# Kernel optimization log

Hardware: AMD Instinct MI355X
Metric: run time of the kernel (lower is better)

Reference implementation:

```python
import jax, jax.numpy as jnp
import numpy as np

TAU = 0.08


def setup_inputs() -> dict:
    key = jax.random.key(0)
    k1, k2 = jax.random.split(key)
    pos_waves = jax.random.normal(k1, (32, 64, 8192), dtype=jnp.float32)
    neg_waves = jax.random.normal(k2, (32, 64, 8192), dtype=jnp.float32)
    return {"pos_waves": pos_waves, "neg_waves": neg_waves}


def _normalize(w):
    # global min/max over the whole wave tensor (matches torch.min/torch.max on 2D tensor)
    lo = jnp.min(w, axis=(1, 2), keepdims=True)  # [N,1,1]
    hi = jnp.max(w, axis=(1, 2), keepdims=True)
    return (w - lo) / (hi - lo)


def _pairwise_negpearson(X, Y):
    # X: [N,B,T], Y: [M,B,T] -> mean over B of (1 - pearson) for every (n,m) pair
    T = X.shape[-1]
    sx = jnp.sum(X, axis=-1)            # [N,B]
    sy = jnp.sum(Y, axis=-1)            # [M,B]
    sx2 = jnp.sum(X * X, axis=-1)       # [N,B]
    sy2 = jnp.sum(Y * Y, axis=-1)       # [M,B]
    sxy = jnp.einsum('nbt,mbt->nmb', X, Y)  # [N,M,B]
    num = T * sxy - sx[:, None, :] * sy[None, :, :]
    den = jnp.sqrt((T * sx2 - sx * sx)[:, None, :] * (T * sy2 - sy * sy)[None, :, :])
    return jnp.mean(1.0 - num / den, axis=-1)  # [N,M]


def reference(pos_waves, neg_waves):
    P = _normalize(pos_waves)   # [N,B,T]
    Q = _normalize(neg_waves)   # [M,B,T]
    N = P.shape[0]

    d_pp = _pairwise_negpearson(P, P)                    # [N,N]
    upper = jnp.triu(jnp.ones((N, N), dtype=bool), k=1)  # i < j pairs only
    pos_total = jnp.sum(jnp.where(upper, jnp.exp(d_pp / TAU), 0.0))

    d_pn = _pairwise_negpearson(P, Q)                    # [N,M]
    neg_total = jnp.sum(jnp.exp(d_pn / TAU))

    return jnp.log10(pos_total / neg_total + 1.0)
```

## Files before the change

### kernel.cpp

```cpp
#include <hip/hip_runtime.h>
#include <cmath>

#define N_ 32
#define B_ 64
#define T_ 8192
#define CPB 16
#define PSTRIDE 2176
#define PAIRF 260
#define TENSF 4160
#define LDSB  33280

typedef _Float16 half8 __attribute__((ext_vector_type(8)));
typedef float floatx4 __attribute__((ext_vector_type(4)));

__global__ __launch_bounds__(512, 8) void k_stage1(const float* __restrict__ pos,
                                                   const float* __restrict__ neg,
                                                   float* __restrict__ partial) {
    __shared__ __align__(16) float smem[LDSB / 4];

    const int bid = blockIdx.x;
    const int b = bid >> 4, c = bid & 15;
    const int tid = threadIdx.x;
    const int wave = tid >> 6, lane = tid & 63;

    const int tzw = wave >> 2;
    const int quad = wave & 3;
    const float* gsrc = tzw ? neg : pos;
    const float* gptr[4];
    int ldsoff[4];
#pragma unroll
    for (int j = 0; j < 4; ++j) {
        int p = quad * 4 + j;
        int row = 2 * p + (lane >> 5);
        gptr[j] = gsrc + ((long)(row * B_ + b)) * T_ + c * 512 + (lane & 31) * 4;
        ldsoff[j] = tzw * TENSF + p * PAIRF;
    }

    const int mat = wave >> 2, qi = (wave >> 1) & 1, qj = wave & 1;
    const int m16 = lane & 15, h2 = lane >> 4;
    const int arow = qi * 16 + m16, brow = qj * 16 + m16;
    const float* aptr = smem + ((arow >> 1) * PAIRF + (arow & 1) * 128);
    const float* bptr = smem + mat * TENSF + ((brow >> 1) * PAIRF + (brow & 1) * 128);

    const int stream = tid >> 3, sub = tid & 7;
    const int srow = stream & 31, stz = stream >> 5;
    const float* sptr = smem + stz * TENSF + ((srow >> 1) * PAIRF + (srow & 1) * 128) + sub * 16;

    floatx4 acc = {};
    float ssum = 0.f, ssq = 0.f;

    for (int ch = 0; ch < 4; ++ch) {
#pragma unroll
        for (int j = 0; j < 4; ++j) {
            __builtin_amdgcn_global_load_lds(
                (const __attribute__((address_space(1))) void*)(gptr[j] + ch * 128),
                (__attribute__((address_space(3))) void*)(smem + ldsoff[j]), 16, 0, 0);
        }
        asm volatile("s_waitcnt vmcnt(0)" ::: "memory");
        __syncthreads();

#pragma unroll
        for (int kk = 0; kk < 4; ++kk) {
            const int t0 = kk * 32 + h2 * 8;
            float4 a0 = *(const float4*)(aptr + t0);
            float4 a1 = *(const float4*)(aptr + t0 + 4);
            float4 b0 = *(const float4*)(bptr + t0);
            float4 b1 = *(const float4*)(bptr + t0 + 4);
            half8 af = {(_Float16)a0.x, (_Float16)a0.y, (_Float16)a0.z, (_Float16)a0.w,
                        (_Float16)a1.x, (_Float16)a1.y, (_Float16)a1.z, (_Float16)a1.w};
            half8 bf = {(_Float16)b0.x, (_Float16)b0.y, (_Float16)b0.z, (_Float16)b0.w,
                        (_Float16)b1.x, (_Float16)b1.y, (_Float16)b1.z, (_Float16)b1.w};
            acc = __builtin_amdgcn_mfma_f32_16x16x32_f16(af, bf, acc, 0, 0, 0);
        }

#pragma unroll
        for (int f = 0; f < 4; ++f) {
            float4 v = *(const float4*)(sptr + f * 4);
            ssum += v.x + v.y + v.z + v.w;
            ssq = fmaf(v.x, v.x, ssq); ssq = fmaf(v.y, v.y, ssq);
            ssq = fmaf(v.z, v.z, ssq); ssq = fmaf(v.w, v.w, ssq);
        }

        __syncthreads();
    }

    ssum += __shfl_xor(ssum, 1); ssum += __shfl_xor(ssum, 2); ssum += __shfl_xor(ssum, 4);
    ssq += __shfl_xor(ssq, 1); ssq += __shfl_xor(ssq, 2); ssq += __shfl_xor(ssq, 4);

    float* out = partial + (long)bid * PSTRIDE;
    if (sub == 0) out[2048 + (stz * 2 + 0) * 32 + srow] = ssum;
    if (sub == 1) out[2048 + (stz * 2 + 1) * 32 + srow] = ssq;

#pragma unroll
    for (int reg = 0; reg < 4; ++reg) {
        int rr = qi * 16 + h2 * 4 + reg;
        int cc = qj * 16 + m16;
        out[mat * 1024 + rr * 32 + cc] = acc[reg];
    }
}

__global__ void k_reduce(const float* __restrict__ partial, float* __restrict__ red) {
    const int b = blockIdx.y;
    const int o = blockIdx.x * 128 + threadIdx.x;
    const float* in = partial + (long)b * CPB * PSTRIDE;
    float s = 0.f;
#pragma unroll
    for (int c = 0; c < CPB; ++c) s += in[c * PSTRIDE + o];
    red[(long)b * PSTRIDE + o] = s;
}

__global__ void k_entries(const float* __restrict__ red, double* __restrict__ blocksums) {
    const int tid = threadIdx.x;
    const int w = tid >> 6, lane = tid & 63;
    const int entry = blockIdx.x * 4 + w;
    const int mat = entry >> 10;
    const int idx = entry & 1023;
    const int n = idx >> 5, m = idx & 31;

    const float* rb = red + (long)lane * PSTRIDE;
    float g = rb[mat * 1024 + idx];
    float sxn = rb[2048 + n];
    float sx2n = rb[2080 + n];
    float sym, sy2m;
    if (mat == 0) {
        sym = rb[2048 + m];
        sy2m = rb[2080 + m];
    } else {
        sym = rb[2112 + m];
        sy2m = rb[2144 + m];
    }

    double num = (double)T_ * (double)g - (double)sxn * (double)sym;
    double vx = (double)T_ * (double)sx2n - (double)sxn * (double)sxn;
    double vy = (double)T_ * (double)sy2m - (double)sym * (double)sym;
    double contrib = 1.0 - num / sqrt(vx * vy);

#pragma unroll
    for (int off = 32; off; off >>= 1) contrib += __shfl_down(contrib, off);

    __shared__ double s_pos[4], s_neg[4];
    if (lane == 0) {
        double d = contrib * (1.0 / B_);
        double term = exp(d / 0.08);
        double p = 0.0, q = 0.0;
        if (mat == 0) {
            if (n < m) p = term;
        } else {
            q = term;
        }
        s_pos[w] = p;
        s_neg[w] = q;
    }
    __syncthreads();
    if (tid == 0) {
        blocksums[blockIdx.x * 2 + 0] = s_pos[0] + s_pos[1] + s_pos[2] + s_pos[3];
        blocksums[blockIdx.x * 2 + 1] = s_neg[0] + s_neg[1] + s_neg[2] + s_neg[3];
    }
}

__global__ void k_final(const double* __restrict__ blocksums, float* __restrict__ out) {
    __shared__ double sp[256], sn[256];
    const int tid = threadIdx.x;
    double p = 0.0, q = 0.0;
    for (int i = tid; i < 512; i += 256) {
        p += blocksums[2 * i + 0];
        q += blocksums[2 * i + 1];
    }
    sp[tid] = p;
    sn[tid] = q;
    __syncthreads();
    for (int s = 128; s; s >>= 1) {
        if (tid < s) {
            sp[tid] += sp[tid + s];
            sn[tid] += sn[tid + s];
        }
        __syncthreads();
    }
    if (tid == 0) out[0] = (float)log10(sp[0] / sn[0] + 1.0);
}

extern "C" void kernel_launch(void* const* d_in, const int* in_sizes, int n_in,
                              void* d_out, int out_size, void* d_ws, size_t ws_size,
                              hipStream_t stream) {
    const float* pos = (const float*)d_in[0];
    const float* neg = (const float*)d_in[1];
    float* out = (float*)d_out;

    char* ws = (char*)d_ws;
    float* partial = (float*)ws;
    float* red = (float*)(ws + (size_t)1024 * PSTRIDE * 4);
    double* blocksums = (double*)(ws + (size_t)1024 * PSTRIDE * 4 + (size_t)64 * PSTRIDE * 4);

    k_stage1<<<1024, 512, 0, stream>>>(pos, neg, partial);
    k_reduce<<<dim3(17, 64), 128, 0, stream>>>(partial, red);
    k_entries<<<512, 256, 0, stream>>>(red, blocksums);
    k_final<<<1, 256, 0, stream>>>(blocksums, out);
}
```

Measured before the change: 167.0 us.

## Double-buffer LDS loads with XOR swizzle and fold row stats into MFMA loop

Stage 1 now processes 1024-sample slices per block (512 blocks, 8 chunks) and double-buffers the global-to-LDS async loads, so the next chunk streams in while MFMA runs on the current one. The padded LDS layout is replaced by an XOR-swizzled layout to avoid bank conflicts. The separate sum and sum-of-squares pass over LDS is folded into the operand reads of selected waves. This halves the partial buffer and the reduce work, at the cost of fewer blocks, lower occupancy (launch bounds 4) and twice the LDS per block.

```diff
diff --git a/kernel.cpp b/kernel.cpp
--- a/kernel.cpp
+++ b/kernel.cpp
@@ -4,68 +4,97 @@
 #define N_ 32
 #define B_ 64
 #define T_ 8192
-#define CPB 16
+#define SLICES 8
+#define NCH 8
 #define PSTRIDE 2176
-#define PAIRF 260
-#define TENSF 4160
-#define LDSB  33280
+#define BUFF 8192
 
 typedef _Float16 half8 __attribute__((ext_vector_type(8)));
 typedef float floatx4 __attribute__((ext_vector_type(4)));
 
-__global__ __launch_bounds__(512, 8) void k_stage1(const float* __restrict__ pos,
+__global__ __launch_bounds__(512, 4) void k_stage1(const float* __restrict__ pos,
                                                    const float* __restrict__ neg,
                                                    float* __restrict__ partial) {
-    __shared__ __align__(16) float smem[LDSB / 4];
+    __shared__ __align__(16) float smem[2 * BUFF];
 
     const int bid = blockIdx.x;
-    const int b = bid >> 4, c = bid & 15;
+    const int b = bid >> 3, c = bid & 7;
     const int tid = threadIdx.x;
     const int wave = tid >> 6, lane = tid & 63;
 
-    const int tzw = wave >> 2;
+    const int tz = wave >> 2;
     const int quad = wave & 3;
-    const float* gsrc = tzw ? neg : pos;
+    const float* gsrc = tz ? neg : pos;
     const float* gptr[4];
-    int ldsoff[4];
+    int dmaoff[4];
 #pragma unroll
     for (int j = 0; j < 4; ++j) {
         int p = quad * 4 + j;
         int row = 2 * p + (lane >> 5);
-        gptr[j] = gsrc + ((long)(row * B_ + b)) * T_ + c * 512 + (lane & 31) * 4;
-        ldsoff[j] = tzw * TENSF + p * PAIRF;
+        int sw = row & 7;
+        int js_src = (lane & 31) ^ sw;
+        gptr[j] = gsrc + ((long)(row * B_ + b)) * T_ + c * 1024 + js_src * 4;
+        dmaoff[j] = tz * 4096 + p * 256;
     }
 
     const int mat = wave >> 2, qi = (wave >> 1) & 1, qj = wave & 1;
     const int m16 = lane & 15, h2 = lane >> 4;
     const int arow = qi * 16 + m16, brow = qj * 16 + m16;
-    const float* aptr = smem + ((arow >> 1) * PAIRF + (arow & 1) * 128);
-    const float* bptr = smem + mat * TENSF + ((brow >> 1) * PAIRF + (brow & 1) * 128);
-
-    const int stream = tid >> 3, sub = tid & 7;
-    const int srow = stream & 31, stz = stream >> 5;
-    const float* sptr = smem + stz * TENSF + ((srow >> 1) * PAIRF + (srow & 1) * 128) + sub * 16;
+    const int aoffb = (arow >> 1) * 256 + (arow & 1) * 128;
+    const int boffb = mat * 4096 + (brow >> 1) * 256 + (brow & 1) * 128;
+    const int swa = arow & 7, swb = brow & 7;
+    const bool statp = (mat == 0) && (qj == 0);
+    const bool statn = (mat == 1) && (qi == 0);
 
     floatx4 acc = {};
     float ssum = 0.f, ssq = 0.f;
 
-    for (int ch = 0; ch < 4; ++ch) {
-#pragma unroll
-        for (int j = 0; j < 4; ++j) {
-            __builtin_amdgcn_global_load_lds(
-                (const __attribute__((address_space(1))) void*)(gptr[j] + ch * 128),
-                (__attribute__((address_space(3))) void*)(smem + ldsoff[j]), 16, 0, 0);
-        }
-        asm volatile("s_waitcnt vmcnt(0)" ::: "memory");
-        __syncthreads();
-
+#define ISSUE(ch, buf)                                                              \
+    do {                                                                            \
+        _Pragma("unroll") for (int j = 0; j < 4; ++j) {                             \
+            __builtin_amdgcn_global_load_lds(                                       \
+                (const __attribute__((address_space(1))) void*)(gptr[j] + (ch)*128),\
+                (__attribute__((address_space(3))) void*)(smem + (buf)*BUFF + dmaoff[j]), \
+                16, 0, 0);                                                          \
+        }                                                                           \
+    } while (0)
+
+    ISSUE(0, 0);
+    ISSUE(1, 1);
+
+    for (int ch = 0; ch < NCH; ++ch) {
+        const int buf = ch & 1;
+        if (ch < NCH - 1) {
+            asm volatile("s_waitcnt vmcnt(4)" ::: "memory");
+        } else {
+            asm volatile("s_waitcnt vmcnt(0)" ::: "memory");
+        }
+        asm volatile("s_barrier" ::: "memory");
+
+        const float* base = smem + buf * BUFF;
 #pragma unroll
         for (int kk = 0; kk < 4; ++kk) {
-            const int t0 = kk * 32 + h2 * 8;
-            float4 a0 = *(const float4*)(aptr + t0);
-            float4 a1 = *(const float4*)(aptr + t0 + 4);
-            float4 b0 = *(const float4*)(bptr + t0);
-            float4 b1 = *(const float4*)(bptr + t0 + 4);
+            const int js = kk * 8 + h2 * 2;
+            float4 a0 = *(const float4*)(base + aoffb + ((js ^ swa) << 2));
+            float4 a1 = *(const float4*)(base + aoffb + (((js + 1) ^ swa) << 2));
+            float4 b0 = *(const float4*)(base + boffb + ((js ^ swb) << 2));
+            float4 b1 = *(const float4*)(base + boffb + (((js + 1) ^ swb) << 2));
+
+            if (statp) {
+                ssum += a0.x + a0.y + a0.z + a0.w + a1.x + a1.y + a1.z + a1.w;
+                ssq = fmaf(a0.x, a0.x, ssq); ssq = fmaf(a0.y, a0.y, ssq);
+                ssq = fmaf(a0.z, a0.z, ssq); ssq = fmaf(a0.w, a0.w, ssq);
+                ssq = fmaf(a1.x, a1.x, ssq); ssq = fmaf(a1.y, a1.y, ssq);
+                ssq = fmaf(a1.z, a1.z, ssq); ssq = fmaf(a1.w, a1.w, ssq);
+            }
+            if (statn) {
+                ssum += b0.x + b0.y + b0.z + b0.w + b1.x + b1.y + b1.z + b1.w;
+                ssq = fmaf(b0.x, b0.x, ssq); ssq = fmaf(b0.y, b0.y, ssq);
+                ssq = fmaf(b0.z, b0.z, ssq); ssq = fmaf(b0.w, b0.w, ssq);
+                ssq = fmaf(b1.x, b1.x, ssq); ssq = fmaf(b1.y, b1.y, ssq);
+                ssq = fmaf(b1.z, b1.z, ssq); ssq = fmaf(b1.w, b1.w, ssq);
+            }
+
             half8 af = {(_Float16)a0.x, (_Float16)a0.y, (_Float16)a0.z, (_Float16)a0.w,
                         (_Float16)a1.x, (_Float16)a1.y, (_Float16)a1.z, (_Float16)a1.w};
             half8 bf = {(_Float16)b0.x, (_Float16)b0.y, (_Float16)b0.z, (_Float16)b0.w,
@@ -73,23 +102,25 @@
             acc = __builtin_amdgcn_mfma_f32_16x16x32_f16(af, bf, acc, 0, 0, 0);
         }
 
-#pragma unroll
-        for (int f = 0; f < 4; ++f) {
-            float4 v = *(const float4*)(sptr + f * 4);
-            ssum += v.x + v.y + v.z + v.w;
-            ssq = fmaf(v.x, v.x, ssq); ssq = fmaf(v.y, v.y, ssq);
-            ssq = fmaf(v.z, v.z, ssq); ssq = fmaf(v.w, v.w, ssq);
-        }
-
-        __syncthreads();
-    }
-
-    ssum += __shfl_xor(ssum, 1); ssum += __shfl_xor(ssum, 2); ssum += __shfl_xor(ssum, 4);
-    ssq += __shfl_xor(ssq, 1); ssq += __shfl_xor(ssq, 2); ssq += __shfl_xor(ssq, 4);
+        asm volatile("s_barrier" ::: "memory");
+        if (ch + 2 < NCH) ISSUE(ch + 2, buf);
+    }
+#undef ISSUE
+
+    ssum += __shfl_xor(ssum, 16); ssum += __shfl_xor(ssum, 32);
+    ssq += __shfl_xor(ssq, 16); ssq += __shfl_xor(ssq, 32);
 
     float* out = partial + (long)bid * PSTRIDE;
-    if (sub == 0) out[2048 + (stz * 2 + 0) * 32 + srow] = ssum;
-    if (sub == 1) out[2048 + (stz * 2 + 1) * 32 + srow] = ssq;
+    if (h2 == 0) {
+        if (statp) {
+            out[2048 + arow] = ssum;
+            out[2080 + arow] = ssq;
+        }
+        if (statn) {
+            out[2112 + brow] = ssum;
+            out[2144 + brow] = ssq;
+        }
+    }
 
 #pragma unroll
     for (int reg = 0; reg < 4; ++reg) {
@@ -102,10 +133,10 @@
 __global__ void k_reduce(const float* __restrict__ partial, float* __restrict__ red) {
     const int b = blockIdx.y;
     const int o = blockIdx.x * 128 + threadIdx.x;
-    const float* in = partial + (long)b * CPB * PSTRIDE;
+    const float* in = partial + (long)b * SLICES * PSTRIDE;
     float s = 0.f;
 #pragma unroll
-    for (int c = 0; c < CPB; ++c) s += in[c * PSTRIDE + o];
+    for (int c = 0; c < SLICES; ++c) s += in[c * PSTRIDE + o];
     red[(long)b * PSTRIDE + o] = s;
 }
 
@@ -188,10 +219,10 @@
 
     char* ws = (char*)d_ws;
     float* partial = (float*)ws;
-    float* red = (float*)(ws + (size_t)1024 * PSTRIDE * 4);
-    double* blocksums = (double*)(ws + (size_t)1024 * PSTRIDE * 4 + (size_t)64 * PSTRIDE * 4);
-
-    k_stage1<<<1024, 512, 0, stream>>>(pos, neg, partial);
+    float* red = (float*)(ws + (size_t)512 * PSTRIDE * 4);
+    double* blocksums = (double*)(ws + (size_t)512 * PSTRIDE * 4 + (size_t)64 * PSTRIDE * 4);
+
+    k_stage1<<<512, 512, 0, stream>>>(pos, neg, partial);
     k_reduce<<<dim3(17, 64), 128, 0, stream>>>(partial, red);
     k_entries<<<512, 256, 0, stream>>>(red, blocksums);
     k_final<<<1, 256, 0, stream>>>(blocksums, out);
```

After: 161.9 us. 1.03x faster.

## Relayout inputs to swizzled FP8 and compute Gram with FP8 MFMA

Applied to the files above, without the earlier changes.

Adds a relayout pass that reads the fp32 waves once, computes per-row sums and sums of squares, and writes the data as FP8 in a per-batch, swizzled layout. A new Gram kernel streams that compact FP8 data through double-buffered LDS and runs fp8 MFMA instead of converting fp32 to fp16 on the fly. The goal is less conversion and LDS work in the hot loop and cheaper reads during the Gram stage. The cost is an extra kernel plus a 32 MB workspace round trip. FP8 precision may be too coarse for the Pearson values, which are amplified by exp(d/0.08).

```diff
diff --git a/kernel.cpp b/kernel.cpp
--- a/kernel.cpp
+++ b/kernel.cpp
@@ -4,109 +4,127 @@
 #define N_ 32
 #define B_ 64
 #define T_ 8192
-#define CPB 16
-#define PSTRIDE 2176
-#define PAIRF 260
-#define TENSF 4160
-#define LDSB  33280
-
-typedef _Float16 half8 __attribute__((ext_vector_type(8)));
+#define REDSTRIDE 2176
+#define PARTSTRIDE 2048
+
 typedef float floatx4 __attribute__((ext_vector_type(4)));
 
-__global__ __launch_bounds__(512, 8) void k_stage1(const float* __restrict__ pos,
-                                                   const float* __restrict__ neg,
-                                                   float* __restrict__ partial) {
-    __shared__ __align__(16) float smem[LDSB / 4];
+__global__ __launch_bounds__(256) void k_relayout(const float* __restrict__ pos,
+                                                  const float* __restrict__ neg,
+                                                  unsigned char* __restrict__ W,
+                                                  float* __restrict__ red) {
+    const int tid = threadIdx.x;
+    const int wave = tid >> 6, lane = tid & 63;
+    const int R = blockIdx.x * 4 + wave;
+    const int tz = R >> 11;
+    const int r = R & 2047;
+    const int n = r >> 6, b = r & 63;
+    const float* src = (tz ? neg : pos) + (long)r * T_ + lane * 4;
+    const int sw = (n & 7) << 1;
+    const int k8 = lane >> 1, sub = lane & 1;
+    unsigned char* dst0 = W + tz * 8192 + n * 256 + ((k8 ^ sw) << 3) + (sub << 2);
+
+    float ssum = 0.f, ssq = 0.f;
+    for (int g = 0; g < 8; ++g) {
+        float4 v[4];
+#pragma unroll
+        for (int u = 0; u < 4; ++u)
+            v[u] = *(const float4*)(src + (g * 4 + u) * 256);
+#pragma unroll
+        for (int u = 0; u < 4; ++u) {
+            const int it = g * 4 + u;
+            const int c = it >> 2, ci = it & 3;
+            float4 x = v[u];
+            ssum += x.x + x.y + x.z + x.w;
+            ssq = fmaf(x.x, x.x, ssq); ssq = fmaf(x.y, x.y, ssq);
+            ssq = fmaf(x.z, x.z, ssq); ssq = fmaf(x.w, x.w, ssq);
+            int pk = __builtin_amdgcn_cvt_pk_fp8_f32(x.x, x.y, 0, false);
+            pk = __builtin_amdgcn_cvt_pk_fp8_f32(x.z, x.w, pk, true);
+            *(int*)(dst0 + (size_t)(((b * 8 + c) * 4 + ci)) * 16384) = pk;
+        }
+    }
+
+    ssum += __shfl_xor(ssum, 1); ssum += __shfl_xor(ssum, 2); ssum += __shfl_xor(ssum, 4);
+    ssum += __shfl_xor(ssum, 8); ssum += __shfl_xor(ssum, 16); ssum += __shfl_xor(ssum, 32);
+    ssq += __shfl_xor(ssq, 1); ssq += __shfl_xor(ssq, 2); ssq += __shfl_xor(ssq, 4);
+    ssq += __shfl_xor(ssq, 8); ssq += __shfl_xor(ssq, 16); ssq += __shfl_xor(ssq, 32);
+    if (lane == 0) {
+        red[(long)b * REDSTRIDE + 2048 + tz * 64 + n] = ssum;
+        red[(long)b * REDSTRIDE + 2048 + tz * 64 + 32 + n] = ssq;
+    }
+}
+
+__global__ __launch_bounds__(512, 4) void k_gram(const unsigned char* __restrict__ W,
+                                                 float* __restrict__ partial) {
+    __shared__ __align__(16) unsigned char smem[2][16384];
 
     const int bid = blockIdx.x;
-    const int b = bid >> 4, c = bid & 15;
     const int tid = threadIdx.x;
     const int wave = tid >> 6, lane = tid & 63;
-
-    const int tzw = wave >> 2;
-    const int quad = wave & 3;
-    const float* gsrc = tzw ? neg : pos;
-    const float* gptr[4];
-    int ldsoff[4];
-#pragma unroll
-    for (int j = 0; j < 4; ++j) {
-        int p = quad * 4 + j;
-        int row = 2 * p + (lane >> 5);
-        gptr[j] = gsrc + ((long)(row * B_ + b)) * T_ + c * 512 + (lane & 31) * 4;
-        ldsoff[j] = tzw * TENSF + p * PAIRF;
-    }
-
     const int mat = wave >> 2, qi = (wave >> 1) & 1, qj = wave & 1;
     const int m16 = lane & 15, h2 = lane >> 4;
     const int arow = qi * 16 + m16, brow = qj * 16 + m16;
-    const float* aptr = smem + ((arow >> 1) * PAIRF + (arow & 1) * 128);
-    const float* bptr = smem + mat * TENSF + ((brow >> 1) * PAIRF + (brow & 1) * 128);
-
-    const int stream = tid >> 3, sub = tid & 7;
-    const int srow = stream & 31, stz = stream >> 5;
-    const float* sptr = smem + stz * TENSF + ((srow >> 1) * PAIRF + (srow & 1) * 128) + sub * 16;
+    const int aoff = arow * 256;
+    const int boff = mat * 8192 + brow * 256;
+    const int swa = (arow & 7) << 1, swb = (brow & 7) << 1;
+    const unsigned char* gsrc = W + (size_t)bid * 65536 + lane * 16;
 
     floatx4 acc = {};
-    float ssum = 0.f, ssq = 0.f;
-
-    for (int ch = 0; ch < 4; ++ch) {
-#pragma unroll
-        for (int j = 0; j < 4; ++j) {
-            __builtin_amdgcn_global_load_lds(
-                (const __attribute__((address_space(1))) void*)(gptr[j] + ch * 128),
-                (__attribute__((address_space(3))) void*)(smem + ldsoff[j]), 16, 0, 0);
-        }
-        asm volatile("s_waitcnt vmcnt(0)" ::: "memory");
-        __syncthreads();
-
-#pragma unroll
-        for (int kk = 0; kk < 4; ++kk) {
-            const int t0 = kk * 32 + h2 * 8;
-            float4 a0 = *(const float4*)(aptr + t0);
-            float4 a1 = *(const float4*)(aptr + t0 + 4);
-            float4 b0 = *(const float4*)(bptr + t0);
-            float4 b1 = *(const float4*)(bptr + t0 + 4);
-            half8 af = {(_Float16)a0.x, (_Float16)a0.y, (_Float16)a0.z, (_Float16)a0.w,
-                        (_Float16)a1.x, (_Float16)a1.y, (_Float16)a1.z, (_Float16)a1.w};
-            half8 bf = {(_Float16)b0.x, (_Float16)b0.y, (_Float16)b0.z, (_Float16)b0.w,
-                        (_Float16)b1.x, (_Float16)b1.y, (_Float16)b1.z, (_Float16)b1.w};
-            acc = __builtin_amdgcn_mfma_f32_16x16x32_f16(af, bf, acc, 0, 0, 0);
-        }
-
-#pragma unroll
-        for (int f = 0; f < 4; ++f) {
-            float4 v = *(const float4*)(sptr + f * 4);
-            ssum += v.x + v.y + v.z + v.w;
-            ssq = fmaf(v.x, v.x, ssq); ssq = fmaf(v.y, v.y, ssq);
-            ssq = fmaf(v.z, v.z, ssq); ssq = fmaf(v.w, v.w, ssq);
-        }
-
-        __syncthreads();
-    }
-
-    ssum += __shfl_xor(ssum, 1); ssum += __shfl_xor(ssum, 2); ssum += __shfl_xor(ssum, 4);
-    ssq += __shfl_xor(ssq, 1); ssq += __shfl_xor(ssq, 2); ssq += __shfl_xor(ssq, 4);
-
-    float* out = partial + (long)bid * PSTRIDE;
-    if (sub == 0) out[2048 + (stz * 2 + 0) * 32 + srow] = ssum;
-    if (sub == 1) out[2048 + (stz * 2 + 1) * 32 + srow] = ssq;
-
+
+#define ISSUE(ci, buf)                                                                \
+    do {                                                                              \
+        _Pragma("unroll") for (int g = 0; g < 2; ++g) {                               \
+            __builtin_amdgcn_global_load_lds(                                         \
+                (const __attribute__((address_space(1))) void*)(gsrc + (ci)*16384 +   \
+                                                                wave * 2048 + g * 1024), \
+                (__attribute__((address_space(3))) void*)(&smem[buf][wave * 2048 + g * 1024]), \
+                16, 0, 0);                                                            \
+        }                                                                             \
+    } while (0)
+
+    ISSUE(0, 0);
+    ISSUE(1, 1);
+
+    for (int ci = 0; ci < 4; ++ci) {
+        const int buf = ci & 1;
+        if (ci < 3) {
+            asm volatile("s_waitcnt vmcnt(2)" ::: "memory");
+        } else {
+            asm volatile("s_waitcnt vmcnt(0)" ::: "memory");
+        }
+        asm volatile("s_barrier" ::: "memory");
+
+        const unsigned char* base = smem[buf];
+#pragma unroll
+        for (int kk = 0; kk < 8; ++kk) {
+            const int u = kk * 4 + h2;
+            long long av = *(const long long*)(base + aoff + ((u ^ swa) << 3));
+            long long bv = *(const long long*)(base + boff + ((u ^ swb) << 3));
+            acc = __builtin_amdgcn_mfma_f32_16x16x32_fp8_fp8(av, bv, acc, 0, 0, 0);
+        }
+
+        asm volatile("s_barrier" ::: "memory");
+        if (ci + 2 < 4) ISSUE(ci + 2, buf);
+    }
+#undef ISSUE
+
+    float* out = partial + (long)bid * PARTSTRIDE + mat * 1024;
 #pragma unroll
     for (int reg = 0; reg < 4; ++reg) {
         int rr = qi * 16 + h2 * 4 + reg;
         int cc = qj * 16 + m16;
-        out[mat * 1024 + rr * 32 + cc] = acc[reg];
+        out[rr * 32 + cc] = acc[reg];
     }
 }
 
 __global__ void k_reduce(const float* __restrict__ partial, float* __restrict__ red) {
     const int b = blockIdx.y;
     const int o = blockIdx.x * 128 + threadIdx.x;
-    const float* in = partial + (long)b * CPB * PSTRIDE;
+    const float* in = partial + (long)b * 8 * PARTSTRIDE;
     float s = 0.f;
 #pragma unroll
-    for (int c = 0; c < CPB; ++c) s += in[c * PSTRIDE + o];
-    red[(long)b * PSTRIDE + o] = s;
+    for (int c = 0; c < 8; ++c) s += in[c * PARTSTRIDE + o];
+    red[(long)b * REDSTRIDE + o] = s;
 }
 
 __global__ void k_entries(const float* __restrict__ red, double* __restrict__ blocksums) {
@@ -117,7 +135,7 @@
     const int idx = entry & 1023;
     const int n = idx >> 5, m = idx & 31;
 
-    const float* rb = red + (long)lane * PSTRIDE;
+    const float* rb = red + (long)lane * REDSTRIDE;
     float g = rb[mat * 1024 + idx];
     float sxn = rb[2048 + n];
     float sx2n = rb[2080 + n];
@@ -187,12 +205,14 @@
     float* out = (float*)d_out;
 
     char* ws = (char*)d_ws;
-    float* partial = (float*)ws;
-    float* red = (float*)(ws + (size_t)1024 * PSTRIDE * 4);
-    double* blocksums = (double*)(ws + (size_t)1024 * PSTRIDE * 4 + (size_t)64 * PSTRIDE * 4);
-
-    k_stage1<<<1024, 512, 0, stream>>>(pos, neg, partial);
-    k_reduce<<<dim3(17, 64), 128, 0, stream>>>(partial, red);
+    unsigned char* W = (unsigned char*)ws;
+    float* partial = (float*)(ws + 33554432);
+    float* red = (float*)(ws + 33554432 + 4194304);
+    double* blocksums = (double*)(ws + 33554432 + 4194304 + 557056);
+
+    k_relayout<<<1024, 256, 0, stream>>>(pos, neg, W, red);
+    k_gram<<<512, 512, 0, stream>>>(W, partial);
+    k_reduce<<<dim3(16, 64), 128, 0, stream>>>(partial, red);
     k_entries<<<512, 256, 0, stream>>>(red, blocksums);
     k_final<<<1, 256, 0, stream>>>(blocksums, out);
 }
```

New measurement: 163.7 us. -2.0%, faster.

## Fuse stats and fp8 conversion in registers, double-buffer LDS with FP8 MFMA

Applied to the files above, without the earlier changes.

Replaces the direct global-to-LDS fp32 staging with register loads. Each thread accumulates the sum and sum-of-squares in fp32, packs values to fp8, and writes them into a swizzled, double-buffered LDS tile consumed by fp8 MFMA. Each block now covers twice as much T, which halves the grid and the partial-reduction work. The aim is to cut LDS traffic and barriers, but fp8 inputs to the cross-product lower accuracy of the correlation, which is then amplified by exp(d/0.08).

```diff
diff --git a/kernel.cpp b/kernel.cpp
--- a/kernel.cpp
+++ b/kernel.cpp
@@ -4,92 +4,87 @@
 #define N_ 32
 #define B_ 64
 #define T_ 8192
-#define CPB 16
+#define SLICES 8
 #define PSTRIDE 2176
-#define PAIRF 260
-#define TENSF 4160
-#define LDSB  33280
 
-typedef _Float16 half8 __attribute__((ext_vector_type(8)));
 typedef float floatx4 __attribute__((ext_vector_type(4)));
 
-__global__ __launch_bounds__(512, 8) void k_stage1(const float* __restrict__ pos,
-                                                   const float* __restrict__ neg,
-                                                   float* __restrict__ partial) {
-    __shared__ __align__(16) float smem[LDSB / 4];
+__global__ __launch_bounds__(512, 4) void k_fused(const float* __restrict__ pos,
+                                                  const float* __restrict__ neg,
+                                                  float* __restrict__ partial) {
+    __shared__ __align__(16) unsigned char smem[2][64 * 512];
 
     const int bid = blockIdx.x;
-    const int b = bid >> 4, c = bid & 15;
+    const int b = bid >> 3, c = bid & 7;
     const int tid = threadIdx.x;
     const int wave = tid >> 6, lane = tid & 63;
 
-    const int tzw = wave >> 2;
-    const int quad = wave & 3;
-    const float* gsrc = tzw ? neg : pos;
-    const float* gptr[4];
-    int ldsoff[4];
-#pragma unroll
-    for (int j = 0; j < 4; ++j) {
-        int p = quad * 4 + j;
-        int row = 2 * p + (lane >> 5);
-        gptr[j] = gsrc + ((long)(row * B_ + b)) * T_ + c * 512 + (lane & 31) * 4;
-        ldsoff[j] = tzw * TENSF + p * PAIRF;
-    }
+    const int R = tid >> 3, sub = tid & 7;
+    const int tz = R >> 5, n = R & 31;
+    const float4* s4 = (const float4*)((tz ? neg : pos) + ((long)(n * B_ + b)) * T_ + c * 1024);
+    const int rsw = R & 15;
 
     const int mat = wave >> 2, qi = (wave >> 1) & 1, qj = wave & 1;
     const int m16 = lane & 15, h2 = lane >> 4;
     const int arow = qi * 16 + m16, brow = qj * 16 + m16;
-    const float* aptr = smem + ((arow >> 1) * PAIRF + (arow & 1) * 128);
-    const float* bptr = smem + mat * TENSF + ((brow >> 1) * PAIRF + (brow & 1) * 128);
-
-    const int stream = tid >> 3, sub = tid & 7;
-    const int srow = stream & 31, stz = stream >> 5;
-    const float* sptr = smem + stz * TENSF + ((srow >> 1) * PAIRF + (srow & 1) * 128) + sub * 16;
+    const int aR = arow, bR = mat * 32 + brow;
+    const int aswz = arow & 15, bswz = brow & 15;
 
     floatx4 acc = {};
     float ssum = 0.f, ssq = 0.f;
+    float4 v[16];
 
-    for (int ch = 0; ch < 4; ++ch) {
-#pragma unroll
-        for (int j = 0; j < 4; ++j) {
-            __builtin_amdgcn_global_load_lds(
-                (const __attribute__((address_space(1))) void*)(gptr[j] + ch * 128),
-                (__attribute__((address_space(3))) void*)(smem + ldsoff[j]), 16, 0, 0);
-        }
-        asm volatile("s_waitcnt vmcnt(0)" ::: "memory");
-        __syncthreads();
+#define LOADCH(ch)                                                   \
+    _Pragma("unroll") for (int i = 0; i < 16; ++i)                   \
+        v[i] = s4[(ch) * 128 + sub + 8 * i];
 
-#pragma unroll
-        for (int kk = 0; kk < 4; ++kk) {
-            const int t0 = kk * 32 + h2 * 8;
-            float4 a0 = *(const float4*)(aptr + t0);
-            float4 a1 = *(const float4*)(aptr + t0 + 4);
-            float4 b0 = *(const float4*)(bptr + t0);
-            float4 b1 = *(const float4*)(bptr + t0 + 4);
-            half8 af = {(_Float16)a0.x, (_Float16)a0.y, (_Float16)a0.z, (_Float16)a0.w,
-                        (_Float16)a1.x, (_Float16)a1.y, (_Float16)a1.z, (_Float16)a1.w};
-            half8 bf = {(_Float16)b0.x, (_Float16)b0.y, (_Float16)b0.z, (_Float16)b0.w,
-                        (_Float16)b1.x, (_Float16)b1.y, (_Float16)b1.z, (_Float16)b1.w};
-            acc = __builtin_amdgcn_mfma_f32_16x16x32_f16(af, bf, acc, 0, 0, 0);
-        }
+#define PROCESS(buf)                                                 \
+    _Pragma("unroll") for (int i = 0; i < 16; ++i) {                 \
+        float4 x = v[i];                                             \
+        ssum += x.x + x.y + x.z + x.w;                               \
+        ssq = fmaf(x.x, x.x, ssq); ssq = fmaf(x.y, x.y, ssq);        \
+        ssq = fmaf(x.z, x.z, ssq); ssq = fmaf(x.w, x.w, ssq);        \
+        int pk = __builtin_amdgcn_cvt_pk_fp8_f32(x.x, x.y, 0, false);\
+        pk = __builtin_amdgcn_cvt_pk_fp8_f32(x.z, x.w, pk, true);    \
+        int f = sub + 8 * i;                                         \
+        int u = f >> 1, hf = f & 1;                                  \
+        int uph = (u & 48) | ((u ^ rsw) & 15);                       \
+        *(int*)&smem[buf][R * 512 + uph * 8 + hf * 4] = pk;          \
+    }
 
-#pragma unroll
-        for (int f = 0; f < 4; ++f) {
-            float4 v = *(const float4*)(sptr + f * 4);
-            ssum += v.x + v.y + v.z + v.w;
-            ssq = fmaf(v.x, v.x, ssq); ssq = fmaf(v.y, v.y, ssq);
-            ssq = fmaf(v.z, v.z, ssq); ssq = fmaf(v.w, v.w, ssq);
-        }
+#define MFMACH(buf)                                                  \
+    _Pragma("unroll") for (int kk = 0; kk < 16; ++kk) {              \
+        int u = kk * 4 + h2;                                         \
+        int ua = (u & 48) | ((u ^ aswz) & 15);                       \
+        int ub = (u & 48) | ((u ^ bswz) & 15);                       \
+        long long av = *(const long long*)&smem[buf][aR * 512 + ua * 8]; \
+        long long bv = *(const long long*)&smem[buf][bR * 512 + ub * 8]; \
+        acc = __builtin_amdgcn_mfma_f32_16x16x32_fp8_fp8(av, bv, acc, 0, 0, 0); \
+    }
 
-        __syncthreads();
-    }
+    LOADCH(0);
+    PROCESS(0);
+    LOADCH(1);
+    asm volatile("s_waitcnt lgkmcnt(0)" ::: "memory");
+    asm volatile("s_barrier" ::: "memory");
+    MFMACH(0);
+    PROCESS(1);
+    asm volatile("s_waitcnt lgkmcnt(0)" ::: "memory");
+    asm volatile("s_barrier" ::: "memory");
+    MFMACH(1);
+
+#undef LOADCH
+#undef PROCESS
+#undef MFMACH
 
     ssum += __shfl_xor(ssum, 1); ssum += __shfl_xor(ssum, 2); ssum += __shfl_xor(ssum, 4);
     ssq += __shfl_xor(ssq, 1); ssq += __shfl_xor(ssq, 2); ssq += __shfl_xor(ssq, 4);
 
     float* out = partial + (long)bid * PSTRIDE;
-    if (sub == 0) out[2048 + (stz * 2 + 0) * 32 + srow] = ssum;
-    if (sub == 1) out[2048 + (stz * 2 + 1) * 32 + srow] = ssq;
+    if (sub == 0) {
+        out[2048 + tz * 64 + n] = ssum;
+        out[2048 + tz * 64 + 32 + n] = ssq;
+    }
 
 #pragma unroll
     for (int reg = 0; reg < 4; ++reg) {
@@ -102,10 +97,10 @@
 __global__ void k_reduce(const float* __restrict__ partial, float* __restrict__ red) {
     const int b = blockIdx.y;
     const int o = blockIdx.x * 128 + threadIdx.x;
-    const float* in = partial + (long)b * CPB * PSTRIDE;
+    const float* in = partial + (long)b * SLICES * PSTRIDE;
     float s = 0.f;
 #pragma unroll
-    for (int c = 0; c < CPB; ++c) s += in[c * PSTRIDE + o];
+    for (int c = 0; c < SLICES; ++c) s += in[c * PSTRIDE + o];
     red[(long)b * PSTRIDE + o] = s;
 }
 
@@ -188,10 +183,10 @@
 
     char* ws = (char*)d_ws;
     float* partial = (float*)ws;
-    float* red = (float*)(ws + (size_t)1024 * PSTRIDE * 4);
-    double* blocksums = (double*)(ws + (size_t)1024 * PSTRIDE * 4 + (size_t)64 * PSTRIDE * 4);
+    float* red = (float*)(ws + (size_t)512 * PSTRIDE * 4);
+    double* blocksums = (double*)(ws + (size_t)512 * PSTRIDE * 4 + (size_t)64 * PSTRIDE * 4);
 
-    k_stage1<<<1024, 512, 0, stream>>>(pos, neg, partial);
+    k_fused<<<512, 512, 0, stream>>>(pos, neg, partial);
     k_reduce<<<dim3(17, 64), 128, 0, stream>>>(partial, red);
     k_entries<<<512, 256, 0, stream>>>(red, blocksums);
     k_final<<<1, 256, 0, stream>>>(blocksums, out);
```

Result: slower. 181.3 us (+8.6%).
